# Optimization experiments

Measured on AMD Instinct MI355X. Metric: run time of the kernel, lower is better.

Reference implementation:

```python
import jax, jax.numpy as jnp
import numpy as np

N_NODES = 100000
N_EDGES = 600000
NUM_GRAPHS = 256
GCN_DIMS = [5, 32, 64, 128, 64, 32]
MLP_DIMS = [32, 32, 16, 1]


def setup_inputs() -> dict:
    key = jax.random.key(0)
    ks = jax.random.split(key, 32)
    inp = {}
    inp["x"] = jax.random.normal(ks[0], (N_NODES, GCN_DIMS[0]), dtype=jnp.float32)
    inp["edge_index"] = jax.random.randint(ks[1], (2, N_EDGES), 0, N_NODES, dtype=jnp.int64)
    inp["edge_attr"] = jax.random.uniform(ks[2], (N_EDGES,), dtype=jnp.float32)
    inp["batch"] = jnp.sort(jax.random.randint(ks[3], (N_NODES,), 0, NUM_GRAPHS, dtype=jnp.int64))
    # GraphConv params: lin_rel (with bias) applied to aggregated messages, lin_root (no bias) to self.
    ki = 4
    for i in range(5):
        fin, fout = GCN_DIMS[i], GCN_DIMS[i + 1]
        s = 1.0 / np.sqrt(fin)
        inp[f"W_rel{i}"] = jax.random.uniform(ks[ki], (fin, fout), jnp.float32, -s, s); ki += 1
        inp[f"b_rel{i}"] = jax.random.uniform(ks[ki], (fout,), jnp.float32, -s, s); ki += 1
        inp[f"W_root{i}"] = jax.random.uniform(ks[ki], (fin, fout), jnp.float32, -s, s); ki += 1
    for i in range(3):
        fin, fout = MLP_DIMS[i], MLP_DIMS[i + 1]
        s = 1.0 / np.sqrt(fin)
        inp[f"mlp_W{i}"] = jax.random.uniform(ks[ki], (fin, fout), jnp.float32, -s, s); ki += 1
        inp[f"mlp_b{i}"] = jax.random.uniform(ks[ki], (fout,), jnp.float32, -s, s); ki += 1
    return inp


def _graph_conv(x, src, dst, w, W_rel, b_rel, W_root):
    # message: x_j * edge_weight, gathered from source nodes
    msg = x[src] * w[:, None]                                  # [E, Fin]
    agg = jax.ops.segment_sum(msg, dst, num_segments=x.shape[0])  # scatter-add -> [N, Fin]
    return agg @ W_rel + b_rel + x @ W_root


def reference(x, edge_index, edge_attr, batch,
              W_rel0, b_rel0, W_root0, W_rel1, b_rel1, W_root1,
              W_rel2, b_rel2, W_root2, W_rel3, b_rel3, W_root3,
              W_rel4, b_rel4, W_root4,
              mlp_W0, mlp_b0, mlp_W1, mlp_b1, mlp_W2, mlp_b2):
    src, dst = edge_index[0], edge_index[1]
    convs = [(W_rel0, b_rel0, W_root0), (W_rel1, b_rel1, W_root1),
             (W_rel2, b_rel2, W_root2), (W_rel3, b_rel3, W_root3),
             (W_rel4, b_rel4, W_root4)]
    for Wr, br, Ws in convs:
        x = jax.nn.relu(_graph_conv(x, src, dst, edge_attr, Wr, br, Ws))
    # global mean pool over graphs
    sums = jax.ops.segment_sum(x, batch, num_segments=NUM_GRAPHS)          # [G, 32]
    cnts = jax.ops.segment_sum(jnp.ones((x.shape[0],), x.dtype), batch, num_segments=NUM_GRAPHS)
    h = sums / jnp.maximum(cnts, 1.0)[:, None]
    mlp = [(mlp_W0, mlp_b0), (mlp_W1, mlp_b1), (mlp_W2, mlp_b2)]
    for i, (W, b) in enumerate(mlp):
        h = h @ W + b
        if i < len(mlp) - 1:
            h = jax.nn.relu(h)
    return h
```

## Files before the change

kernel.cpp:

```cpp
#include <hip/hip_runtime.h>

#define N_NODES 100000
#define N_EDGES 600000
#define NUM_GRAPHS 256

#define SCAN_BS   256
#define SCAN_CH   4
#define SCAN_CHUNK (SCAN_BS * SCAN_CH)
#define SCAN_NB   ((N_NODES + SCAN_CHUNK - 1) / SCAN_CHUNK)

__global__ void hist_kernel(const int* __restrict__ dst, int* __restrict__ deg) {
    int e = blockIdx.x * blockDim.x + threadIdx.x;
    if (e < N_EDGES) atomicAdd(&deg[dst[e]], 1);
}

__global__ void scan_p1_kernel(const int* __restrict__ deg, int* __restrict__ bsum) {
    __shared__ int sh[SCAN_BS];
    const int b = blockIdx.x, t = threadIdx.x;
    const int base = b * SCAN_CHUNK + t * SCAN_CH;
    int s = 0;
    #pragma unroll
    for (int k = 0; k < SCAN_CH; ++k) {
        int i = base + k;
        if (i < N_NODES) s += deg[i];
    }
    sh[t] = s;
    __syncthreads();
    for (int off = SCAN_BS / 2; off > 0; off >>= 1) {
        if (t < off) sh[t] += sh[t + off];
        __syncthreads();
    }
    if (t == 0) bsum[b] = sh[0];
}

__global__ void scan_p2_kernel(int* __restrict__ bsum, int* __restrict__ rowptr) {
    __shared__ int sh[128];
    const int t = threadIdx.x;
    int v = (t < SCAN_NB) ? bsum[t] : 0;
    sh[t] = v;
    __syncthreads();
    for (int off = 1; off < 128; off <<= 1) {
        int u = (t >= off) ? sh[t - off] : 0;
        __syncthreads();
        sh[t] += u;
        __syncthreads();
    }
    if (t < SCAN_NB) bsum[t] = sh[t] - v;
    if (t == 0) rowptr[N_NODES] = N_EDGES;
}

__global__ void scan_p3_kernel(const int* __restrict__ deg, const int* __restrict__ bsum,
                               int* __restrict__ rowptr, int* __restrict__ cursor) {
    __shared__ int sh[SCAN_BS];
    const int b = blockIdx.x, t = threadIdx.x;
    const int base = b * SCAN_CHUNK + t * SCAN_CH;
    int v[SCAN_CH];
    int s = 0;
    #pragma unroll
    for (int k = 0; k < SCAN_CH; ++k) {
        int i = base + k;
        v[k] = (i < N_NODES) ? deg[i] : 0;
        s += v[k];
    }
    sh[t] = s;
    __syncthreads();
    for (int off = 1; off < SCAN_BS; off <<= 1) {
        int u = (t >= off) ? sh[t - off] : 0;
        __syncthreads();
        sh[t] += u;
        __syncthreads();
    }
    int run = bsum[b] + sh[t] - s;
    #pragma unroll
    for (int k = 0; k < SCAN_CH; ++k) {
        int i = base + k;
        if (i < N_NODES) { rowptr[i] = run; cursor[i] = run; }
        run += v[k];
    }
}

__global__ void fill_kernel(const int* __restrict__ src, const int* __restrict__ dst,
                            const float* __restrict__ w, int* __restrict__ cursor,
                            int* __restrict__ ssrc, float* __restrict__ sw) {
    int e = blockIdx.x * blockDim.x + threadIdx.x;
    if (e >= N_EDGES) return;
    int pos = atomicAdd(&cursor[dst[e]], 1);
    ssrc[pos] = src[e];
    sw[pos] = w[e];
}

template<int F, bool FUSED>
__global__ void gather_kernel(const int* __restrict__ rowptr, const int* __restrict__ ssrc,
                              const float* __restrict__ sw, const float* __restrict__ y,
                              const float* __restrict__ r, const float* __restrict__ b,
                              float* __restrict__ out) {
    constexpr int G = F / 4;
    constexpr int NPB = 256 / G;
    const int tid = threadIdx.x;
    const int c = tid % G;
    const int ln = tid / G;
    const int n = blockIdx.x * NPB + ln;
    if (n >= N_NODES) return;
    const int beg = rowptr[n], end = rowptr[n + 1];
    float4 acc = {0.f, 0.f, 0.f, 0.f};
    int i = beg;
    for (; i + 1 < end; i += 2) {
        int s0 = ssrc[i], s1 = ssrc[i + 1];
        float w0 = sw[i], w1 = sw[i + 1];
        float4 v0 = *(reinterpret_cast<const float4*>(y + (size_t)s0 * F) + c);
        float4 v1 = *(reinterpret_cast<const float4*>(y + (size_t)s1 * F) + c);
        acc.x += v0.x * w0 + v1.x * w1;
        acc.y += v0.y * w0 + v1.y * w1;
        acc.z += v0.z * w0 + v1.z * w1;
        acc.w += v0.w * w0 + v1.w * w1;
    }
    if (i < end) {
        int s0 = ssrc[i];
        float w0 = sw[i];
        float4 v0 = *(reinterpret_cast<const float4*>(y + (size_t)s0 * F) + c);
        acc.x += v0.x * w0; acc.y += v0.y * w0; acc.z += v0.z * w0; acc.w += v0.w * w0;
    }
    if constexpr (FUSED) {
        float4 rv = *(reinterpret_cast<const float4*>(r + (size_t)n * F) + c);
        float4 bv = *(reinterpret_cast<const float4*>(b) + c);
        acc.x = fmaxf(acc.x + rv.x + bv.x, 0.f);
        acc.y = fmaxf(acc.y + rv.y + bv.y, 0.f);
        acc.z = fmaxf(acc.z + rv.z + bv.z, 0.f);
        acc.w = fmaxf(acc.w + rv.w + bv.w, 0.f);
    }
    *(reinterpret_cast<float4*>(out + (size_t)n * F) + c) = acc;
}

__global__ void gather5_kernel(const int* __restrict__ rowptr, const int* __restrict__ ssrc,
                               const float* __restrict__ sw, const float* __restrict__ x,
                               float* __restrict__ agg) {
    int n = blockIdx.x * blockDim.x + threadIdx.x;
    if (n >= N_NODES) return;
    float a0 = 0.f, a1 = 0.f, a2 = 0.f, a3 = 0.f, a4 = 0.f;
    for (int i = rowptr[n]; i < rowptr[n + 1]; ++i) {
        int s = ssrc[i];
        float we = sw[i];
        const float* xs = x + (size_t)s * 5;
        a0 += xs[0] * we; a1 += xs[1] * we; a2 += xs[2] * we;
        a3 += xs[3] * we; a4 += xs[4] * we;
    }
    float* o = agg + (size_t)n * 5;
    o[0] = a0; o[1] = a1; o[2] = a2; o[3] = a3; o[4] = a4;
}

template<int FIN, int FOUT, bool DUAL>
__global__ __launch_bounds__(256, 2)
void gemm_kernel(const float* __restrict__ in1, const float* __restrict__ in2,
                 const float* __restrict__ Wrel, const float* __restrict__ Wroot,
                 const float* __restrict__ brel,
                 float* __restrict__ out1, float* __restrict__ out2) {
    constexpr int JG = DUAL ? (FOUT / 2) : (FOUT / 4);
    constexpr int NG = 256 / JG;
    constexpr int TN = NG * 8;
    constexpr int CH = FIN / 4;
    constexpr int TOT = TN * CH;

    __shared__ float smem[(DUAL ? 1 : 2) * TN * FIN];
    float* S1 = smem;
    float* S2 = smem + TN * FIN;

    const int tid = threadIdx.x;
    const int n0 = blockIdx.x * TN;
    const bool full = (n0 + TN <= N_NODES);

    if (full) {
        #pragma unroll
        for (int r = 0; r < TOT / 256; ++r) {
            int idx = r * 256 + tid;
            int n = idx / CH, c = idx - n * CH;
            *(float4*)(S1 + n * FIN + c * 4) =
                *(const float4*)(in1 + (size_t)(n0 + n) * FIN + c * 4);
            if constexpr (!DUAL)
                *(float4*)(S2 + n * FIN + c * 4) =
                    *(const float4*)(in2 + (size_t)(n0 + n) * FIN + c * 4);
        }
    } else {
        #pragma unroll
        for (int r = 0; r < TOT / 256; ++r) {
            int idx = r * 256 + tid;
            int n = idx / CH, c = idx - n * CH;
            float4 z = {0.f, 0.f, 0.f, 0.f};
            bool ok = (n0 + n) < N_NODES;
            *(float4*)(S1 + n * FIN + c * 4) =
                ok ? *(const float4*)(in1 + (size_t)(n0 + n) * FIN + c * 4) : z;
            if constexpr (!DUAL)
                *(float4*)(S2 + n * FIN + c * 4) =
                    ok ? *(const float4*)(in2 + (size_t)(n0 + n) * FIN + c * 4) : z;
        }
    }
    __syncthreads();

    const int jg = tid % JG;
    const int ng = tid / JG;
    const float* sA = S1 + (ng * 8) * FIN;
    const float* sX = S2 + (ng * 8) * FIN;

    const float* Wd = Wrel;
    float* outd = out1;
    int col;
    if constexpr (DUAL) {
        const bool second = jg >= (FOUT / 4);
        Wd = second ? Wroot : Wrel;
        outd = second ? out2 : out1;
        col = (second ? jg - FOUT / 4 : jg) * 4;
    } else {
        col = jg * 4;
    }

    float acc[8][4] = {};

    #pragma unroll 4
    for (int k0 = 0; k0 < FIN; k0 += 4) {
        float a[8][4];
        #pragma unroll
        for (int i = 0; i < 8; ++i) {
            float4 t = *(const float4*)(sA + i * FIN + k0);
            a[i][0] = t.x; a[i][1] = t.y; a[i][2] = t.z; a[i][3] = t.w;
        }
        #pragma unroll
        for (int kk = 0; kk < 4; ++kk) {
            float4 w = *(const float4*)(Wd + (size_t)(k0 + kk) * FOUT + col);
            float wv[4] = {w.x, w.y, w.z, w.w};
            #pragma unroll
            for (int i = 0; i < 8; ++i)
                #pragma unroll
                for (int j = 0; j < 4; ++j)
                    acc[i][j] += a[i][kk] * wv[j];
        }
        if constexpr (!DUAL) {
            #pragma unroll
            for (int i = 0; i < 8; ++i) {
                float4 t = *(const float4*)(sX + i * FIN + k0);
                a[i][0] = t.x; a[i][1] = t.y; a[i][2] = t.z; a[i][3] = t.w;
            }
            #pragma unroll
            for (int kk = 0; kk < 4; ++kk) {
                float4 w = *(const float4*)(Wroot + (size_t)(k0 + kk) * FOUT + col);
                float wv[4] = {w.x, w.y, w.z, w.w};
                #pragma unroll
                for (int i = 0; i < 8; ++i)
                    #pragma unroll
                    for (int j = 0; j < 4; ++j)
                        acc[i][j] += a[i][kk] * wv[j];
            }
        }
    }

    if constexpr (DUAL) {
        #pragma unroll
        for (int i = 0; i < 8; ++i) {
            int n = n0 + ng * 8 + i;
            if (full || n < N_NODES) {
                float4 o = {acc[i][0], acc[i][1], acc[i][2], acc[i][3]};
                *(float4*)(outd + (size_t)n * FOUT + col) = o;
            }
        }
    } else {
        float4 b4 = *(const float4*)(brel + col);
        #pragma unroll
        for (int i = 0; i < 8; ++i) {
            int n = n0 + ng * 8 + i;
            if (full || n < N_NODES) {
                float4 o = {fmaxf(acc[i][0] + b4.x, 0.f), fmaxf(acc[i][1] + b4.y, 0.f),
                            fmaxf(acc[i][2] + b4.z, 0.f), fmaxf(acc[i][3] + b4.w, 0.f)};
                *(float4*)(out1 + (size_t)n * FOUT + col) = o;
            }
        }
    }
}

template<int FIN, int FOUT>
__global__ void conv_out_kernel(const float* __restrict__ agg, const float* __restrict__ x,
                                const float* __restrict__ Wrel, const float* __restrict__ brel,
                                const float* __restrict__ Wroot, float* __restrict__ out) {
    constexpr int JG = FOUT / 4;
    constexpr int NG = 256 / JG;
    constexpr int NT = NG * 4;
    const int tid = threadIdx.x;
    const int jg = tid % JG;
    const int ng = tid / JG;
    const int n0 = blockIdx.x * NT + ng * 4;

    float acc[4][4] = {};
    for (int k = 0; k < FIN; ++k) {
        float a[4], xx[4];
        #pragma unroll
        for (int i = 0; i < 4; ++i) {
            int n = n0 + i;
            a[i]  = (n < N_NODES) ? agg[(size_t)n * FIN + k] : 0.f;
            xx[i] = (n < N_NODES) ? x[(size_t)n * FIN + k]   : 0.f;
        }
        float4 wr = *reinterpret_cast<const float4*>(Wrel  + (size_t)k * FOUT + jg * 4);
        float4 wo = *reinterpret_cast<const float4*>(Wroot + (size_t)k * FOUT + jg * 4);
        float wrv[4] = {wr.x, wr.y, wr.z, wr.w};
        float wov[4] = {wo.x, wo.y, wo.z, wo.w};
        #pragma unroll
        for (int i = 0; i < 4; ++i)
            #pragma unroll
            for (int j = 0; j < 4; ++j)
                acc[i][j] += a[i] * wrv[j] + xx[i] * wov[j];
    }
    float4 b4 = *reinterpret_cast<const float4*>(brel + jg * 4);
    float bv[4] = {b4.x, b4.y, b4.z, b4.w};
    #pragma unroll
    for (int i = 0; i < 4; ++i) {
        int n = n0 + i;
        if (n < N_NODES) {
            #pragma unroll
            for (int j = 0; j < 4; ++j)
                out[(size_t)n * FOUT + jg * 4 + j] = fmaxf(acc[i][j] + bv[j], 0.f);
        }
    }
}

__global__ void pool_mlp_kernel(const float* __restrict__ x, const int* __restrict__ batch,
                                const float* __restrict__ W0, const float* __restrict__ b0,
                                const float* __restrict__ W1, const float* __restrict__ b1,
                                const float* __restrict__ W2, const float* __restrict__ b2,
                                float* __restrict__ out) {
    const int g = blockIdx.x;
    auto lb = [&](int key) {
        int lo = 0, hi = N_NODES;
        while (lo < hi) {
            int mid = (lo + hi) >> 1;
            if (batch[mid] < key) lo = mid + 1; else hi = mid;
        }
        return lo;
    };
    const int beg = lb(g), end = lb(g + 1);

    const int t = threadIdx.x;
    const int q = t & 7;
    const int r = t >> 3;

    float4 s = {0.f, 0.f, 0.f, 0.f};
    for (int n = beg + r; n < end; n += 32) {
        float4 v = *(reinterpret_cast<const float4*>(x + (size_t)n * 32) + q);
        s.x += v.x; s.y += v.y; s.z += v.z; s.w += v.w;
    }
    __shared__ float4 red[32][8];
    red[r][q] = s;
    __syncthreads();

    __shared__ float h0[32], h1[32], h2[16];
    if (r == 0) {
        float4 tot = {0.f, 0.f, 0.f, 0.f};
        #pragma unroll
        for (int i = 0; i < 32; ++i) {
            float4 v = red[i][q];
            tot.x += v.x; tot.y += v.y; tot.z += v.z; tot.w += v.w;
        }
        float c = fmaxf((float)(end - beg), 1.0f);
        h0[q * 4 + 0] = tot.x / c;
        h0[q * 4 + 1] = tot.y / c;
        h0[q * 4 + 2] = tot.z / c;
        h0[q * 4 + 3] = tot.w / c;
    }
    __syncthreads();
    if (t < 32) {
        float s1 = b0[t];
        for (int k = 0; k < 32; ++k) s1 += h0[k] * W0[k * 32 + t];
        h1[t] = fmaxf(s1, 0.f);
    }
    __syncthreads();
    if (t < 16) {
        float s2 = b1[t];
        for (int k = 0; k < 32; ++k) s2 += h1[k] * W1[k * 16 + t];
        h2[t] = fmaxf(s2, 0.f);
    }
    __syncthreads();
    if (t == 0) {
        float s3 = b2[0];
        for (int k = 0; k < 16; ++k) s3 += h2[k] * W2[k];
        out[g] = s3;
    }
}

extern "C" void kernel_launch(void* const* d_in, const int* in_sizes, int n_in,
                              void* d_out, int out_size, void* d_ws, size_t ws_size,
                              hipStream_t stream) {
    const float* x_in  = (const float*)d_in[0];
    const int*   ei    = (const int*)d_in[1];
    const int*   src   = ei;
    const int*   dst   = ei + N_EDGES;
    const float* ew    = (const float*)d_in[2];
    const int*   batch = (const int*)d_in[3];

    const float* Wrel[5]  = {(const float*)d_in[4],  (const float*)d_in[7],  (const float*)d_in[10],
                             (const float*)d_in[13], (const float*)d_in[16]};
    const float* brel[5]  = {(const float*)d_in[5],  (const float*)d_in[8],  (const float*)d_in[11],
                             (const float*)d_in[14], (const float*)d_in[17]};
    const float* Wroot[5] = {(const float*)d_in[6],  (const float*)d_in[9],  (const float*)d_in[12],
                             (const float*)d_in[15], (const float*)d_in[18]};
    const float* mW0 = (const float*)d_in[19];
    const float* mb0 = (const float*)d_in[20];
    const float* mW1 = (const float*)d_in[21];
    const float* mb1 = (const float*)d_in[22];
    const float* mW2 = (const float*)d_in[23];
    const float* mb2 = (const float*)d_in[24];

    float* ws = (float*)d_ws;
    float* A = ws;
    float* B = A + (size_t)N_NODES * 64;
    float* C = B + (size_t)N_NODES * 128;
    int*   rowptr = (int*)(C + (size_t)N_NODES * 64);
    int*   cursor = rowptr + (N_NODES + 2);
    int*   deg    = cursor + N_NODES;
    int*   bsum   = deg + N_NODES;
    int*   ssrc   = bsum + 128;
    float* sw     = (float*)(ssrc + N_EDGES);

    const int BS = 256;
    auto blocks = [](long long total, int bs) { return (int)((total + bs - 1) / bs); };

    hipMemsetAsync(deg, 0, N_NODES * sizeof(int), stream);
    hist_kernel<<<blocks(N_EDGES, BS), BS, 0, stream>>>(dst, deg);
    scan_p1_kernel<<<SCAN_NB, SCAN_BS, 0, stream>>>(deg, bsum);
    scan_p2_kernel<<<1, 128, 0, stream>>>(bsum, rowptr);
    scan_p3_kernel<<<SCAN_NB, SCAN_BS, 0, stream>>>(deg, bsum, rowptr, cursor);
    fill_kernel<<<blocks(N_EDGES, BS), BS, 0, stream>>>(src, dst, ew, cursor, ssrc, sw);

    const int G64  = (N_NODES + 63) / 64;
    const int G128 = (N_NODES + 127) / 128;

    gather5_kernel<<<blocks(N_NODES, BS), BS, 0, stream>>>(rowptr, ssrc, sw, x_in, C);
    conv_out_kernel<5, 32><<<blocks(N_NODES, 128), BS, 0, stream>>>(C, x_in, Wrel[0], brel[0], Wroot[0], B);

    gather_kernel<32, false><<<blocks(N_NODES, 32), BS, 0, stream>>>(rowptr, ssrc, sw, B, nullptr, nullptr, C);
    gemm_kernel<32, 64, false><<<G128, 256, 0, stream>>>(C, B, Wrel[1], Wroot[1], brel[1], A, nullptr);

    gather_kernel<64, false><<<blocks(N_NODES, 16), BS, 0, stream>>>(rowptr, ssrc, sw, A, nullptr, nullptr, C);
    gemm_kernel<64, 128, false><<<G64, 256, 0, stream>>>(C, A, Wrel[2], Wroot[2], brel[2], B, nullptr);

    gemm_kernel<128, 64, true><<<G64, 256, 0, stream>>>(B, nullptr, Wrel[3], Wroot[3], nullptr, C, A);
    gather_kernel<64, true><<<blocks(N_NODES, 16), BS, 0, stream>>>(rowptr, ssrc, sw, C, A, brel[3], B);

    gemm_kernel<64, 32, true><<<G128, 256, 0, stream>>>(B, nullptr, Wrel[4], Wroot[4], nullptr, C, A);
    gather_kernel<32, true><<<blocks(N_NODES, 32), BS, 0, stream>>>(rowptr, ssrc, sw, C, A, brel[4], B);

    pool_mlp_kernel<<<NUM_GRAPHS, 256, 0, stream>>>(B, batch, mW0, mb0, mW1, mb1, mW2, mb2, (float*)d_out);
}
```

Before: 391.6 us.

## Concatenate GEMM inputs along K and software-pipeline register loads in gemm kernel

Stores the rel and root inputs side by side in one shared tile so the non-dual GEMM runs a single K loop of length 2*FIN, with the weight pointer switching halves at FIN. The inner loop is rewritten as a manually double-buffered, non-unrolled loop that loads the next A and W fragments while the current ones are consumed. Launch bounds are raised to three blocks per SM to push occupancy up. The intent is to hide shared and global load latency and cut instruction overhead, at the cost of register pressure under the tighter launch bound.

```diff
diff --git a/kernel.cpp b/kernel.cpp
--- a/kernel.cpp
+++ b/kernel.cpp
@@ -149,107 +149,102 @@
 }
 
 template<int FIN, int FOUT, bool DUAL>
-__global__ __launch_bounds__(256, 2)
+__global__ __launch_bounds__(256, 3)
 void gemm_kernel(const float* __restrict__ in1, const float* __restrict__ in2,
                  const float* __restrict__ Wrel, const float* __restrict__ Wroot,
                  const float* __restrict__ brel,
                  float* __restrict__ out1, float* __restrict__ out2) {
+    constexpr int KT = DUAL ? FIN : 2 * FIN;
     constexpr int JG = DUAL ? (FOUT / 2) : (FOUT / 4);
     constexpr int NG = 256 / JG;
     constexpr int TN = NG * 8;
-    constexpr int CH = FIN / 4;
+    constexpr int CH = KT / 4;
+    constexpr int C1 = FIN / 4;
     constexpr int TOT = TN * CH;
 
-    __shared__ float smem[(DUAL ? 1 : 2) * TN * FIN];
-    float* S1 = smem;
-    float* S2 = smem + TN * FIN;
+    __shared__ float smem[TN * KT];
 
     const int tid = threadIdx.x;
     const int n0 = blockIdx.x * TN;
     const bool full = (n0 + TN <= N_NODES);
 
-    if (full) {
-        #pragma unroll
-        for (int r = 0; r < TOT / 256; ++r) {
-            int idx = r * 256 + tid;
-            int n = idx / CH, c = idx - n * CH;
-            *(float4*)(S1 + n * FIN + c * 4) =
-                *(const float4*)(in1 + (size_t)(n0 + n) * FIN + c * 4);
-            if constexpr (!DUAL)
-                *(float4*)(S2 + n * FIN + c * 4) =
-                    *(const float4*)(in2 + (size_t)(n0 + n) * FIN + c * 4);
-        }
-    } else {
-        #pragma unroll
-        for (int r = 0; r < TOT / 256; ++r) {
-            int idx = r * 256 + tid;
-            int n = idx / CH, c = idx - n * CH;
-            float4 z = {0.f, 0.f, 0.f, 0.f};
-            bool ok = (n0 + n) < N_NODES;
-            *(float4*)(S1 + n * FIN + c * 4) =
-                ok ? *(const float4*)(in1 + (size_t)(n0 + n) * FIN + c * 4) : z;
-            if constexpr (!DUAL)
-                *(float4*)(S2 + n * FIN + c * 4) =
-                    ok ? *(const float4*)(in2 + (size_t)(n0 + n) * FIN + c * 4) : z;
-        }
+    #pragma unroll
+    for (int r2 = 0; r2 < TOT / 256; ++r2) {
+        int idx = r2 * 256 + tid;
+        int n = idx / CH, c = idx - n * CH;
+        int gn = n0 + n;
+        float4 v = {0.f, 0.f, 0.f, 0.f};
+        if (full || gn < N_NODES) {
+            if constexpr (DUAL) {
+                v = *(const float4*)(in1 + (size_t)gn * FIN + c * 4);
+            } else {
+                v = (c < C1) ? *(const float4*)(in1 + (size_t)gn * FIN + c * 4)
+                             : *(const float4*)(in2 + (size_t)gn * FIN + (c - C1) * 4);
+            }
+        }
+        *(float4*)(smem + n * KT + c * 4) = v;
     }
     __syncthreads();
 
     const int jg = tid % JG;
     const int ng = tid / JG;
-    const float* sA = S1 + (ng * 8) * FIN;
-    const float* sX = S2 + (ng * 8) * FIN;
-
-    const float* Wd = Wrel;
+    const float* sA = smem + (ng * 8) * KT;
+
+    const float* pW1;
+    const float* pW2;
     float* outd = out1;
     int col;
     if constexpr (DUAL) {
         const bool second = jg >= (FOUT / 4);
-        Wd = second ? Wroot : Wrel;
+        pW1 = second ? Wroot : Wrel;
+        pW2 = pW1;
         outd = second ? out2 : out1;
         col = (second ? jg - FOUT / 4 : jg) * 4;
     } else {
+        pW1 = Wrel;
+        pW2 = Wroot - (ptrdiff_t)FIN * FOUT;
         col = jg * 4;
     }
 
     float acc[8][4] = {};
-
-    #pragma unroll 4
-    for (int k0 = 0; k0 < FIN; k0 += 4) {
-        float a[8][4];
-        #pragma unroll
-        for (int i = 0; i < 8; ++i) {
-            float4 t = *(const float4*)(sA + i * FIN + k0);
-            a[i][0] = t.x; a[i][1] = t.y; a[i][2] = t.z; a[i][3] = t.w;
-        }
-        #pragma unroll
-        for (int kk = 0; kk < 4; ++kk) {
-            float4 w = *(const float4*)(Wd + (size_t)(k0 + kk) * FOUT + col);
-            float wv[4] = {w.x, w.y, w.z, w.w};
-            #pragma unroll
-            for (int i = 0; i < 8; ++i)
-                #pragma unroll
-                for (int j = 0; j < 4; ++j)
-                    acc[i][j] += a[i][kk] * wv[j];
-        }
-        if constexpr (!DUAL) {
-            #pragma unroll
-            for (int i = 0; i < 8; ++i) {
-                float4 t = *(const float4*)(sX + i * FIN + k0);
-                a[i][0] = t.x; a[i][1] = t.y; a[i][2] = t.z; a[i][3] = t.w;
-            }
-            #pragma unroll
-            for (int kk = 0; kk < 4; ++kk) {
-                float4 w = *(const float4*)(Wroot + (size_t)(k0 + kk) * FOUT + col);
-                float wv[4] = {w.x, w.y, w.z, w.w};
-                #pragma unroll
-                for (int i = 0; i < 8; ++i)
-                    #pragma unroll
-                    for (int j = 0; j < 4; ++j)
-                        acc[i][j] += a[i][kk] * wv[j];
-            }
-        }
-    }
+    float4 aA[8], aB[8], wA[4], wB[4];
+
+    auto wrow = [&](int k) -> float4 {
+        const float* base = (DUAL || k < FIN) ? pW1 : pW2;
+        return *(const float4*)(base + (ptrdiff_t)k * FOUT + col);
+    };
+
+#define LOADT(A_, W_, K0)                                         \
+    { _Pragma("unroll") for (int i = 0; i < 8; ++i)               \
+          A_[i] = *(const float4*)(sA + i * KT + (K0));           \
+      W_[0] = wrow((K0) + 0); W_[1] = wrow((K0) + 1);             \
+      W_[2] = wrow((K0) + 2); W_[3] = wrow((K0) + 3); }
+
+#define FMAT(A_, W_)                                                        \
+    { _Pragma("unroll") for (int i = 0; i < 8; ++i) {                       \
+        acc[i][0] += A_[i].x * W_[0].x; acc[i][1] += A_[i].x * W_[0].y;     \
+        acc[i][2] += A_[i].x * W_[0].z; acc[i][3] += A_[i].x * W_[0].w;     \
+        acc[i][0] += A_[i].y * W_[1].x; acc[i][1] += A_[i].y * W_[1].y;     \
+        acc[i][2] += A_[i].y * W_[1].z; acc[i][3] += A_[i].y * W_[1].w;     \
+        acc[i][0] += A_[i].z * W_[2].x; acc[i][1] += A_[i].z * W_[2].y;     \
+        acc[i][2] += A_[i].z * W_[2].z; acc[i][3] += A_[i].z * W_[2].w;     \
+        acc[i][0] += A_[i].w * W_[3].x; acc[i][1] += A_[i].w * W_[3].y;     \
+        acc[i][2] += A_[i].w * W_[3].z; acc[i][3] += A_[i].w * W_[3].w; } }
+
+    LOADT(aA, wA, 0);
+    LOADT(aB, wB, 4);
+    #pragma unroll 1
+    for (int k0 = 0; k0 < KT - 8; k0 += 8) {
+        FMAT(aA, wA);
+        LOADT(aA, wA, k0 + 8);
+        FMAT(aB, wB);
+        LOADT(aB, wB, k0 + 12);
+    }
+    FMAT(aA, wA);
+    FMAT(aB, wB);
+
+#undef LOADT
+#undef FMAT
 
     if constexpr (DUAL) {
         #pragma unroll
```

New measurement: 362.4 us. 7.5% less time.
